# Kernel optimization log

Hardware: AMD Instinct MI355X
Metric: run time of the kernel (lower is better)

Reference implementation:

```python
import jax, jax.numpy as jnp
import numpy as np

B, D = 131072, 128


def setup_inputs() -> dict:
    key = jax.random.key(0)
    ks = jax.random.split(key, 6)
    return {
        "v": jax.random.normal(ks[0], (B, D), dtype=jnp.float32),
        "e": jax.random.normal(ks[1], (B, D), dtype=jnp.float32),
        "w_vv": jax.random.normal(ks[2], (D,), dtype=jnp.float32),
        "w_ev": jax.random.normal(ks[3], (D,), dtype=jnp.float32),
        "w_ve": jax.random.normal(ks[4], (D,), dtype=jnp.float32),
        "w_ee": jax.random.normal(ks[5], (D,), dtype=jnp.float32),
        "b_v": jnp.zeros((D,), dtype=jnp.float32),
        "b_e": jnp.zeros((D,), dtype=jnp.float32),
    }


def reference(v, e, w_vv, w_ev, w_ve, w_ee, b_v, b_e):
    # C = v e^T  (rank-1), so:
    #   C  @ w      = v * (e . w)
    #   C^T @ w     = e * (v . w)
    # This computes the exact same math as materializing the [B, d, d]
    # outer product and applying the rank-1 Linear projections.
    e_dot_vv = e @ w_vv  # [B]
    v_dot_ev = v @ w_ev  # [B]
    e_dot_ve = e @ w_ve  # [B]
    v_dot_ee = v @ w_ee  # [B]
    v_out = v * e_dot_vv[:, None] + e * v_dot_ev[:, None] + b_v
    e_out = v * e_dot_ve[:, None] + e * v_dot_ee[:, None] + b_e
    return (v_out, e_out)
```

## Files before the change

kernel.cpp:

```cpp
#include <hip/hip_runtime.h>


#define CCU_D 128
#define ROWS_PER_GROUP 4

__device__ __forceinline__ float dot4(const float4 a, const float4 b) {
    return a.x * b.x + a.y * b.y + a.z * b.z + a.w * b.w;
}

__global__ __launch_bounds__(256) void ccu_kernel(
    const float* __restrict__ v,
    const float* __restrict__ e,
    const float* __restrict__ w_vv,
    const float* __restrict__ w_ev,
    const float* __restrict__ w_ve,
    const float* __restrict__ w_ee,
    const float* __restrict__ b_v,
    const float* __restrict__ b_e,
    float* __restrict__ v_out,
    float* __restrict__ e_out,
    int nrows)
{
    const int lane32 = threadIdx.x & 31;
    const int group  = (int)((blockIdx.x * (size_t)blockDim.x + threadIdx.x) >> 5);
    const int base   = group * ROWS_PER_GROUP;
    if (base >= nrows) return;

    const float4 wvv = ((const float4*)w_vv)[lane32];
    const float4 wev = ((const float4*)w_ev)[lane32];
    const float4 wve = ((const float4*)w_ve)[lane32];
    const float4 wee = ((const float4*)w_ee)[lane32];

    float4 vr[ROWS_PER_GROUP], er[ROWS_PER_GROUP];
    #pragma unroll
    for (int k = 0; k < ROWS_PER_GROUP; ++k) {
        vr[k] = ((const float4*)(v + (size_t)(base + k) * CCU_D))[lane32];
        er[k] = ((const float4*)(e + (size_t)(base + k) * CCU_D))[lane32];
    }

    float dvv[ROWS_PER_GROUP], dev[ROWS_PER_GROUP];
    float dve[ROWS_PER_GROUP], dee[ROWS_PER_GROUP];
    #pragma unroll
    for (int k = 0; k < ROWS_PER_GROUP; ++k) {
        dvv[k] = dot4(er[k], wvv);
        dev[k] = dot4(vr[k], wev);
        dve[k] = dot4(er[k], wve);
        dee[k] = dot4(vr[k], wee);
    }

    #pragma unroll
    for (int off = 16; off >= 1; off >>= 1) {
        #pragma unroll
        for (int k = 0; k < ROWS_PER_GROUP; ++k) {
            dvv[k] += __shfl_xor(dvv[k], off);
            dev[k] += __shfl_xor(dev[k], off);
            dve[k] += __shfl_xor(dve[k], off);
            dee[k] += __shfl_xor(dee[k], off);
        }
    }

    const float4 bv = ((const float4*)b_v)[lane32];
    const float4 be = ((const float4*)b_e)[lane32];

    #pragma unroll
    for (int k = 0; k < ROWS_PER_GROUP; ++k) {
        float4 vo, eo;
        vo.x = vr[k].x * dvv[k] + er[k].x * dev[k] + bv.x;
        vo.y = vr[k].y * dvv[k] + er[k].y * dev[k] + bv.y;
        vo.z = vr[k].z * dvv[k] + er[k].z * dev[k] + bv.z;
        vo.w = vr[k].w * dvv[k] + er[k].w * dev[k] + bv.w;

        eo.x = vr[k].x * dve[k] + er[k].x * dee[k] + be.x;
        eo.y = vr[k].y * dve[k] + er[k].y * dee[k] + be.y;
        eo.z = vr[k].z * dve[k] + er[k].z * dee[k] + be.z;
        eo.w = vr[k].w * dve[k] + er[k].w * dee[k] + be.w;

        ((float4*)(v_out + (size_t)(base + k) * CCU_D))[lane32] = vo;
        ((float4*)(e_out + (size_t)(base + k) * CCU_D))[lane32] = eo;
    }
}

extern "C" void kernel_launch(void* const* d_in, const int* in_sizes, int n_in,
                              void* d_out, int out_size, void* d_ws, size_t ws_size,
                              hipStream_t stream) {
    const float* v    = (const float*)d_in[0];
    const float* e    = (const float*)d_in[1];
    const float* w_vv = (const float*)d_in[2];
    const float* w_ev = (const float*)d_in[3];
    const float* w_ve = (const float*)d_in[4];
    const float* w_ee = (const float*)d_in[5];
    const float* b_v  = (const float*)d_in[6];
    const float* b_e  = (const float*)d_in[7];

    const int nrows = in_sizes[0] / CCU_D;
    float* v_out = (float*)d_out;
    float* e_out = (float*)d_out + (size_t)nrows * CCU_D;

    const int rows_per_block = (256 / 32) * ROWS_PER_GROUP;
    const int blocks = (nrows + rows_per_block - 1) / rows_per_block;
    ccu_kernel<<<blocks, 256, 0, stream>>>(v, e, w_vv, w_ev, w_ve, w_ee,
                                           b_v, b_e, v_out, e_out, nrows);
}
```

Measured before the change: 246.5 us.

## Split fused kernel into separate dot-product and apply kernels via workspace

Replaces the single fused kernel with two launches. The first computes the four per-row dot products and writes them as a float4 per row to workspace. The second re-reads v and e and applies the rank-1 update elementwise with one float4 per thread. This aims at more parallelism and simpler kernels, but it reads v and e twice and adds a second launch plus a workspace round trip on a memory-bound op.

```diff
diff --git a/kernel.cpp b/kernel.cpp
--- a/kernel.cpp
+++ b/kernel.cpp
@@ -2,28 +2,25 @@
 
 
 #define CCU_D 128
-#define ROWS_PER_GROUP 4
+#define K1_ROWS 2
 
 __device__ __forceinline__ float dot4(const float4 a, const float4 b) {
     return a.x * b.x + a.y * b.y + a.z * b.z + a.w * b.w;
 }
 
-__global__ __launch_bounds__(256) void ccu_kernel(
+__global__ __launch_bounds__(256) void ccu_dots(
     const float* __restrict__ v,
     const float* __restrict__ e,
     const float* __restrict__ w_vv,
     const float* __restrict__ w_ev,
     const float* __restrict__ w_ve,
     const float* __restrict__ w_ee,
-    const float* __restrict__ b_v,
-    const float* __restrict__ b_e,
-    float* __restrict__ v_out,
-    float* __restrict__ e_out,
+    float4* __restrict__ dots,
     int nrows)
 {
     const int lane32 = threadIdx.x & 31;
     const int group  = (int)((blockIdx.x * (size_t)blockDim.x + threadIdx.x) >> 5);
-    const int base   = group * ROWS_PER_GROUP;
+    const int base   = group * K1_ROWS;
     if (base >= nrows) return;
 
     const float4 wvv = ((const float4*)w_vv)[lane32];
@@ -31,17 +28,16 @@
     const float4 wve = ((const float4*)w_ve)[lane32];
     const float4 wee = ((const float4*)w_ee)[lane32];
 
-    float4 vr[ROWS_PER_GROUP], er[ROWS_PER_GROUP];
+    float4 vr[K1_ROWS], er[K1_ROWS];
     #pragma unroll
-    for (int k = 0; k < ROWS_PER_GROUP; ++k) {
+    for (int k = 0; k < K1_ROWS; ++k) {
         vr[k] = ((const float4*)(v + (size_t)(base + k) * CCU_D))[lane32];
         er[k] = ((const float4*)(e + (size_t)(base + k) * CCU_D))[lane32];
     }
 
-    float dvv[ROWS_PER_GROUP], dev[ROWS_PER_GROUP];
-    float dve[ROWS_PER_GROUP], dee[ROWS_PER_GROUP];
+    float dvv[K1_ROWS], dev[K1_ROWS], dve[K1_ROWS], dee[K1_ROWS];
     #pragma unroll
-    for (int k = 0; k < ROWS_PER_GROUP; ++k) {
+    for (int k = 0; k < K1_ROWS; ++k) {
         dvv[k] = dot4(er[k], wvv);
         dev[k] = dot4(vr[k], wev);
         dve[k] = dot4(er[k], wve);
@@ -51,7 +47,7 @@
     #pragma unroll
     for (int off = 16; off >= 1; off >>= 1) {
         #pragma unroll
-        for (int k = 0; k < ROWS_PER_GROUP; ++k) {
+        for (int k = 0; k < K1_ROWS; ++k) {
             dvv[k] += __shfl_xor(dvv[k], off);
             dev[k] += __shfl_xor(dev[k], off);
             dve[k] += __shfl_xor(dve[k], off);
@@ -59,25 +55,50 @@
         }
     }
 
-    const float4 bv = ((const float4*)b_v)[lane32];
-    const float4 be = ((const float4*)b_e)[lane32];
+    if (lane32 == 0) {
+        #pragma unroll
+        for (int k = 0; k < K1_ROWS; ++k) {
+            float4 d;
+            d.x = dvv[k]; d.y = dev[k]; d.z = dve[k]; d.w = dee[k];
+            dots[base + k] = d;
+        }
+    }
+}
 
-    #pragma unroll
-    for (int k = 0; k < ROWS_PER_GROUP; ++k) {
-        float4 vo, eo;
-        vo.x = vr[k].x * dvv[k] + er[k].x * dev[k] + bv.x;
-        vo.y = vr[k].y * dvv[k] + er[k].y * dev[k] + bv.y;
-        vo.z = vr[k].z * dvv[k] + er[k].z * dev[k] + bv.z;
-        vo.w = vr[k].w * dvv[k] + er[k].w * dev[k] + bv.w;
+__global__ __launch_bounds__(256) void ccu_apply(
+    const float* __restrict__ v,
+    const float* __restrict__ e,
+    const float4* __restrict__ dots,
+    const float* __restrict__ b_v,
+    const float* __restrict__ b_e,
+    float* __restrict__ v_out,
+    float* __restrict__ e_out,
+    int nvec4)
+{
+    const int g = (int)(blockIdx.x * (size_t)blockDim.x + threadIdx.x);
+    if (g >= nvec4) return;
+    const int c   = g & 31;
+    const int row = g >> 5;
 
-        eo.x = vr[k].x * dve[k] + er[k].x * dee[k] + be.x;
-        eo.y = vr[k].y * dve[k] + er[k].y * dee[k] + be.y;
-        eo.z = vr[k].z * dve[k] + er[k].z * dee[k] + be.z;
-        eo.w = vr[k].w * dve[k] + er[k].w * dee[k] + be.w;
+    const float4 vr = ((const float4*)v)[g];
+    const float4 er = ((const float4*)e)[g];
+    const float4 d  = dots[row];
+    const float4 bv = ((const float4*)b_v)[c];
+    const float4 be = ((const float4*)b_e)[c];
 
-        ((float4*)(v_out + (size_t)(base + k) * CCU_D))[lane32] = vo;
-        ((float4*)(e_out + (size_t)(base + k) * CCU_D))[lane32] = eo;
-    }
+    float4 vo, eo;
+    vo.x = vr.x * d.x + er.x * d.y + bv.x;
+    vo.y = vr.y * d.x + er.y * d.y + bv.y;
+    vo.z = vr.z * d.x + er.z * d.y + bv.z;
+    vo.w = vr.w * d.x + er.w * d.y + bv.w;
+
+    eo.x = vr.x * d.z + er.x * d.w + be.x;
+    eo.y = vr.y * d.z + er.y * d.w + be.y;
+    eo.z = vr.z * d.z + er.z * d.w + be.z;
+    eo.w = vr.w * d.z + er.w * d.w + be.w;
+
+    ((float4*)v_out)[g] = vo;
+    ((float4*)e_out)[g] = eo;
 }
 
 extern "C" void kernel_launch(void* const* d_in, const int* in_sizes, int n_in,
@@ -95,9 +116,15 @@
     const int nrows = in_sizes[0] / CCU_D;
     float* v_out = (float*)d_out;
     float* e_out = (float*)d_out + (size_t)nrows * CCU_D;
+    float4* dots = (float4*)d_ws;
 
-    const int rows_per_block = (256 / 32) * ROWS_PER_GROUP;
-    const int blocks = (nrows + rows_per_block - 1) / rows_per_block;
-    ccu_kernel<<<blocks, 256, 0, stream>>>(v, e, w_vv, w_ev, w_ve, w_ee,
-                                           b_v, b_e, v_out, e_out, nrows);
+    const int k1_rows_per_block = (256 / 32) * K1_ROWS;
+    const int k1_blocks = (nrows + k1_rows_per_block - 1) / k1_rows_per_block;
+    ccu_dots<<<k1_blocks, 256, 0, stream>>>(v, e, w_vv, w_ev, w_ve, w_ee,
+                                            dots, nrows);
+
+    const int nvec4 = nrows * (CCU_D / 4);
+    const int k2_blocks = (nvec4 + 255) / 256;
+    ccu_apply<<<k2_blocks, 256, 0, stream>>>(v, e, dots, b_v, b_e,
+                                             v_out, e_out, nvec4);
 }
```

Measured after the change: 259.2 us. 1.05x slower.
